# Performance work log

Hardware: AMD Instinct MI355X
Metric: run time of the kernel (lower is better)

The kernel has to match this reference:

```python
import jax, jax.numpy as jnp
import numpy as np

N = 200000          # active voxels
C = 128             # channels (in == out, required by final elementwise multiply)
GRID = (256, 256, 64)
EPS = 1e-5


def setup_inputs() -> dict:
    rng = np.random.default_rng(0)
    total = GRID[0] * GRID[1] * GRID[2]
    lin = rng.choice(total, size=N, replace=False)
    coords = np.stack(np.unravel_index(lin, GRID), axis=1).astype(np.int64)  # [N,3]
    # dense voxel -> row lookup table; sentinel N means 'no active voxel here'
    lut = np.full(total, N, dtype=np.int32)
    lut[lin] = np.arange(N, dtype=np.int32)
    nb = np.full((3, 2, N), N, dtype=np.int32)  # [axis, {prev,next}, N]
    hi = np.array(GRID) - 1
    for a in range(3):
        for s, off in enumerate((-1, 1)):
            c = coords.copy()
            c[:, a] += off
            valid = (c[:, a] >= 0) & (c[:, a] <= hi[a])
            cc = np.clip(c, 0, hi)
            lin_n = np.ravel_multi_index(tuple(cc.T), GRID)
            nb[a, s] = np.where(valid, lut[lin_n], N)
    kf, kw, kg, kb = jax.random.split(jax.random.key(0), 4)
    features = jax.random.normal(kf, (N, C), jnp.float32)
    W = jax.random.normal(kw, (3, 3, C, C), jnp.float32) * (1.0 / np.sqrt(3.0 * C))
    gamma = 1.0 + 0.1 * jax.random.normal(kg, (3, C), jnp.float32)
    beta = 0.1 * jax.random.normal(kb, (3, C), jnp.float32)
    return {"features": features, "nb_idx": jnp.asarray(nb), "W": W,
            "gamma": gamma, "beta": beta}


def reference(features, nb_idx, W, gamma, beta):
    # zero pad row: gathering sentinel index N yields a zero contribution
    xp = jnp.concatenate([features, jnp.zeros((1, C), features.dtype)], axis=0)
    acc = jnp.zeros_like(features)
    for a in range(3):  # three 1D decomposition axes (3x1x1, 1x3x1, 1x1x3)
        prev = xp[nb_idx[a, 0]]                      # [N,C]
        nxt = xp[nb_idx[a, 1]]                       # [N,C]
        out = prev @ W[a, 0] + features @ W[a, 1] + nxt @ W[a, 2]
        # BatchNorm1d (training-mode batch stats, biased variance)
        mu = out.mean(axis=0)
        var = out.var(axis=0)
        out = (out - mu) * jax.lax.rsqrt(var + EPS) * gamma[a] + beta[a]
        acc = acc + jax.nn.sigmoid(out)
    return acc * features
```

## Files before the change

kernel.cpp:

```cpp
#include <hip/hip_runtime.h>
#include <hip/hip_bf16.h>

#define NVOX 200000
#define CCH  128
#define KTOT 384
#define EPS_BN 1e-5f
#define PB   625
#define TPB  5

typedef __bf16 bf16x8 __attribute__((ext_vector_type(8)));
typedef float  floatx4 __attribute__((ext_vector_type(4)));

#define XBF_OFF    0ull
#define XBF_BYTES  ((size_t)(NVOX + 1) * CCH * 2)
#define WT_OFF     (XBF_OFF + XBF_BYTES)
#define WT_BYTES   ((size_t)3 * CCH * KTOT * 2)
#define OUTB_OFF   (WT_OFF + WT_BYTES)
#define OUTB_BYTES ((size_t)3 * NVOX * CCH * 2)
#define STATS_OFF  (OUTB_OFF + OUTB_BYTES)
#define STATS_BYTES ((size_t)3 * 2 * CCH * 4)

__global__ void k_prep_x(const float* __restrict__ xf, __bf16* __restrict__ xbf) {
    int idx = blockIdx.x * blockDim.x + threadIdx.x;
    const int total = (NVOX + 1) * 16;
    if (idx >= total) return;
    float v[8];
    if (idx < NVOX * 16) {
        const float4* p = (const float4*)xf + (size_t)idx * 2;
        float4 f0 = p[0], f1 = p[1];
        v[0] = f0.x; v[1] = f0.y; v[2] = f0.z; v[3] = f0.w;
        v[4] = f1.x; v[5] = f1.y; v[6] = f1.z; v[7] = f1.w;
    } else {
        #pragma unroll
        for (int j = 0; j < 8; ++j) v[j] = 0.0f;
    }
    bf16x8 o;
    #pragma unroll
    for (int j = 0; j < 8; ++j) o[j] = (__bf16)v[j];
    *((bf16x8*)xbf + idx) = o;
}

__global__ void k_prep_w(const float* __restrict__ W, __bf16* __restrict__ wt) {
    int idx = blockIdx.x * blockDim.x + threadIdx.x;
    if (idx >= 3 * CCH * KTOT) return;
    int k = idx % KTOT; int rem = idx / KTOT;
    int c = rem % CCH;  int a = rem / CCH;
    int s = k >> 7, k0 = k & 127;
    wt[idx] = (__bf16)W[(((size_t)(a * 3 + s) * CCH) + k0) * CCH + c];
}

__launch_bounds__(256, 2)
__global__ void k_gemm(const __bf16* __restrict__ xbf, const __bf16* __restrict__ wt,
                       const int* __restrict__ nb, __bf16* __restrict__ outb,
                       float* __restrict__ stats) {
    __shared__ __bf16 smem[64 * 392];
    __shared__ int s_pn[128];

    const int a    = blockIdx.y;
    const int tid  = threadIdx.x;
    const int w    = tid >> 6;
    const int lane = tid & 63;
    const int q    = lane >> 4;
    const int ln   = lane & 15;

    const __bf16* wbase = wt + (size_t)a * CCH * KTOT;
    bf16x8 B0[12], B1[12];
    #pragma unroll
    for (int ks = 0; ks < 12; ++ks) {
        B0[ks] = *(const bf16x8*)(wbase + (size_t)(w * 32 + ln) * KTOT + ks * 32 + q * 8);
        B1[ks] = *(const bf16x8*)(wbase + (size_t)(w * 32 + 16 + ln) * KTOT + ks * 32 + q * 8);
    }

    for (int ti = 0; ti < TPB; ++ti) {
        const int row0 = (blockIdx.x + ti * PB) * 64;

        __syncthreads();
        if (tid < 128)
            s_pn[tid] = nb[(size_t)(a * 2 + (tid >> 6)) * NVOX + row0 + (tid & 63)];
        __syncthreads();

        bf16x8 areg[12];
        #pragma unroll
        for (int it = 0; it < 12; ++it) {
            int cc  = it * 256 + tid;
            int r   = cc / 48;
            int seg = cc - r * 48;
            int src = seg >> 4, ch = seg & 15;
            int g = (src == 1) ? (row0 + r) : s_pn[(src >> 1) * 64 + r];
            areg[it] = *(const bf16x8*)(xbf + (size_t)g * CCH + ch * 8);
        }
        #pragma unroll
        for (int it = 0; it < 12; ++it) {
            int cc  = it * 256 + tid;
            int r   = cc / 48;
            int seg = cc - r * 48;
            *(bf16x8*)(&smem[r * 392 + seg * 8]) = areg[it];
        }
        __syncthreads();

        floatx4 acc0[4], acc1[4];
        #pragma unroll
        for (int mt = 0; mt < 4; ++mt)
            #pragma unroll
            for (int r = 0; r < 4; ++r) { acc0[mt][r] = 0.0f; acc1[mt][r] = 0.0f; }

        #pragma unroll
        for (int ks = 0; ks < 12; ++ks) {
            #pragma unroll
            for (int mt = 0; mt < 4; ++mt) {
                bf16x8 afr = *(const bf16x8*)(&smem[(mt * 16 + ln) * 392 + ks * 32 + q * 8]);
                acc0[mt] = __builtin_amdgcn_mfma_f32_16x16x32_bf16(afr, B0[ks], acc0[mt], 0, 0, 0);
                acc1[mt] = __builtin_amdgcn_mfma_f32_16x16x32_bf16(afr, B1[ks], acc1[mt], 0, 0, 0);
            }
        }

        {
            float s0 = 0.f, ss0 = 0.f, s1 = 0.f, ss1 = 0.f;
            #pragma unroll
            for (int mt = 0; mt < 4; ++mt)
                #pragma unroll
                for (int r = 0; r < 4; ++r) {
                    float v0 = acc0[mt][r]; s0 += v0; ss0 += v0 * v0;
                    float v1 = acc1[mt][r]; s1 += v1; ss1 += v1 * v1;
                }
            s0 += __shfl_xor(s0, 16); ss0 += __shfl_xor(ss0, 16);
            s0 += __shfl_xor(s0, 32); ss0 += __shfl_xor(ss0, 32);
            s1 += __shfl_xor(s1, 16); ss1 += __shfl_xor(ss1, 16);
            s1 += __shfl_xor(s1, 32); ss1 += __shfl_xor(ss1, 32);
            if (lane < 16) {
                int c0 = w * 32 + lane, c1 = w * 32 + 16 + lane;
                atomicAdd(&stats[a * 2 * CCH + c0], s0);
                atomicAdd(&stats[a * 2 * CCH + CCH + c0], ss0);
                atomicAdd(&stats[a * 2 * CCH + c1], s1);
                atomicAdd(&stats[a * 2 * CCH + CCH + c1], ss1);
            }
        }

        __syncthreads();
        #pragma unroll
        for (int mt = 0; mt < 4; ++mt) {
            #pragma unroll
            for (int r = 0; r < 4; ++r) {
                int rr = mt * 16 + q * 4 + r;
                smem[rr * 136 + w * 32 + ln]      = (__bf16)acc0[mt][r];
                smem[rr * 136 + w * 32 + 16 + ln] = (__bf16)acc1[mt][r];
            }
        }
        __syncthreads();
        #pragma unroll
        for (int it = 0; it < 4; ++it) {
            int i = it * 256 + tid;
            int r = i >> 4, ch = i & 15;
            bf16x8 v = *(const bf16x8*)(&smem[r * 136 + ch * 8]);
            *(bf16x8*)(outb + ((size_t)a * NVOX + row0 + r) * CCH + ch * 8) = v;
        }
    }
}

__launch_bounds__(256)
__global__ void k_final(const __bf16* __restrict__ outb, const float* __restrict__ xf,
                        const float* __restrict__ stats, const float* __restrict__ gamma,
                        const float* __restrict__ beta, float* __restrict__ out) {
    __shared__ float lsc[384], lsh[384];
    int tid = threadIdx.x;
    for (int i = tid; i < 384; i += 256) {
        int a = i >> 7, c = i & 127;
        float mu  = stats[a * 256 + c] * (1.0f / NVOX);
        float var = stats[a * 256 + 128 + c] * (1.0f / NVOX) - mu * mu;
        float rs  = rsqrtf(var + EPS_BN);
        float g = gamma[i], b = beta[i];
        lsc[i] = rs * g;
        lsh[i] = b - mu * rs * g;
    }
    __syncthreads();
    const int total = NVOX * 16;
    for (int idx = blockIdx.x * 256 + tid; idx < total; idx += gridDim.x * 256) {
        int c0 = (idx & 15) * 8;
        float4 f0 = ((const float4*)xf)[(size_t)idx * 2];
        float4 f1 = ((const float4*)xf)[(size_t)idx * 2 + 1];
        float r[8];
        #pragma unroll
        for (int j = 0; j < 8; ++j) r[j] = 0.0f;
        #pragma unroll
        for (int a = 0; a < 3; ++a) {
            bf16x8 o = *((const bf16x8*)outb + (size_t)a * NVOX * 16 + idx);
            #pragma unroll
            for (int j = 0; j < 8; ++j) {
                float v = (float)o[j] * lsc[a * 128 + c0 + j] + lsh[a * 128 + c0 + j];
                r[j] += __builtin_amdgcn_rcpf(1.0f + __expf(-v));
            }
        }
        float4 o0, o1;
        o0.x = r[0] * f0.x; o0.y = r[1] * f0.y; o0.z = r[2] * f0.z; o0.w = r[3] * f0.w;
        o1.x = r[4] * f1.x; o1.y = r[5] * f1.y; o1.z = r[6] * f1.z; o1.w = r[7] * f1.w;
        ((float4*)out)[(size_t)idx * 2]     = o0;
        ((float4*)out)[(size_t)idx * 2 + 1] = o1;
    }
}

extern "C" void kernel_launch(void* const* d_in, const int* in_sizes, int n_in,
                              void* d_out, int out_size, void* d_ws, size_t ws_size,
                              hipStream_t stream) {
    const float* xf    = (const float*)d_in[0];
    const int*   nb    = (const int*)  d_in[1];
    const float* W     = (const float*)d_in[2];
    const float* gamma = (const float*)d_in[3];
    const float* beta  = (const float*)d_in[4];
    float* out = (float*)d_out;

    char* ws = (char*)d_ws;
    __bf16* xbf   = (__bf16*)(ws + XBF_OFF);
    __bf16* wt    = (__bf16*)(ws + WT_OFF);
    __bf16* outb  = (__bf16*)(ws + OUTB_OFF);
    float*  stats = (float*)(ws + STATS_OFF);

    hipMemsetAsync(stats, 0, STATS_BYTES, stream);
    k_prep_x<<<((NVOX + 1) * 16 + 255) / 256, 256, 0, stream>>>(xf, xbf);
    k_prep_w<<<(3 * CCH * KTOT + 255) / 256, 256, 0, stream>>>(W, wt);
    k_gemm<<<dim3(PB, 3), 256, 0, stream>>>(xbf, wt, nb, outb, stats);
    k_final<<<2048, 256, 0, stream>>>(outb, xf, stats, gamma, beta, out);
}
```

Measured before the change: 415.5 us.

## Prefetch next tile's gathered rows during MFMA and defer BN stat atomics

```diff
diff --git a/kernel.cpp b/kernel.cpp
--- a/kernel.cpp
+++ b/kernel.cpp
@@ -53,8 +53,9 @@
 __global__ void k_gemm(const __bf16* __restrict__ xbf, const __bf16* __restrict__ wt,
                        const int* __restrict__ nb, __bf16* __restrict__ outb,
                        float* __restrict__ stats) {
-    __shared__ __bf16 smem[64 * 392];
-    __shared__ int s_pn[128];
+    __shared__ __bf16 smemA[64 * 392];
+    __shared__ __bf16 smemO[64 * 136];
+    __shared__ int s_pn[2][128];
 
     const int a    = blockIdx.y;
     const int tid  = threadIdx.x;
@@ -71,33 +72,63 @@
         B1[ks] = *(const bf16x8*)(wbase + (size_t)(w * 32 + 16 + ln) * KTOT + ks * 32 + q * 8);
     }
 
-    for (int ti = 0; ti < TPB; ++ti) {
-        const int row0 = (blockIdx.x + ti * PB) * 64;
-
-        __syncthreads();
-        if (tid < 128)
-            s_pn[tid] = nb[(size_t)(a * 2 + (tid >> 6)) * NVOX + row0 + (tid & 63)];
-        __syncthreads();
-
-        bf16x8 areg[12];
+    float s0 = 0.f, ss0 = 0.f, s1 = 0.f, ss1 = 0.f;
+
+    int r_pn = 0;
+    if (tid < 128) {
+        r_pn = nb[(size_t)(a * 2 + (tid >> 6)) * NVOX + blockIdx.x * 64 + (tid & 63)];
+        s_pn[0][tid] = r_pn;
+    }
+    __syncthreads();
+
+    bf16x8 areg[12];
+    {
+        const int row0 = blockIdx.x * 64;
         #pragma unroll
         for (int it = 0; it < 12; ++it) {
             int cc  = it * 256 + tid;
             int r   = cc / 48;
             int seg = cc - r * 48;
             int src = seg >> 4, ch = seg & 15;
-            int g = (src == 1) ? (row0 + r) : s_pn[(src >> 1) * 64 + r];
+            int g = (src == 1) ? (row0 + r) : s_pn[0][(src >> 1) * 64 + r];
             areg[it] = *(const bf16x8*)(xbf + (size_t)g * CCH + ch * 8);
         }
+    }
+    if (tid < 128)
+        r_pn = nb[(size_t)(a * 2 + (tid >> 6)) * NVOX + (blockIdx.x + PB) * 64 + (tid & 63)];
+
+    #pragma unroll
+    for (int ti = 0; ti < TPB; ++ti) {
+        const int row0 = (blockIdx.x + ti * PB) * 64;
+        const int buf  = ti & 1;
+
         #pragma unroll
         for (int it = 0; it < 12; ++it) {
             int cc  = it * 256 + tid;
             int r   = cc / 48;
             int seg = cc - r * 48;
-            *(bf16x8*)(&smem[r * 392 + seg * 8]) = areg[it];
-        }
+            *(bf16x8*)(&smemA[r * 392 + seg * 8]) = areg[it];
+        }
+        if (ti + 1 < TPB && tid < 128) s_pn[buf ^ 1][tid] = r_pn;
         __syncthreads();
 
+        bf16x8 areg2[12];
+        if (ti + 1 < TPB) {
+            const int rown = (blockIdx.x + (ti + 1) * PB) * 64;
+            #pragma unroll
+            for (int it = 0; it < 12; ++it) {
+                int cc  = it * 256 + tid;
+                int r   = cc / 48;
+                int seg = cc - r * 48;
+                int src = seg >> 4, ch = seg & 15;
+                int g = (src == 1) ? (rown + r) : s_pn[buf ^ 1][(src >> 1) * 64 + r];
+                areg2[it] = *(const bf16x8*)(xbf + (size_t)g * CCH + ch * 8);
+            }
+            if (ti + 2 < TPB && tid < 128)
+                r_pn = nb[(size_t)(a * 2 + (tid >> 6)) * NVOX
+                          + (blockIdx.x + (ti + 2) * PB) * 64 + (tid & 63)];
+        }
+
         floatx4 acc0[4], acc1[4];
         #pragma unroll
         for (int mt = 0; mt < 4; ++mt)
@@ -108,52 +139,55 @@
         for (int ks = 0; ks < 12; ++ks) {
             #pragma unroll
             for (int mt = 0; mt < 4; ++mt) {
-                bf16x8 afr = *(const bf16x8*)(&smem[(mt * 16 + ln) * 392 + ks * 32 + q * 8]);
+                bf16x8 afr = *(const bf16x8*)(&smemA[(mt * 16 + ln) * 392 + ks * 32 + q * 8]);
                 acc0[mt] = __builtin_amdgcn_mfma_f32_16x16x32_bf16(afr, B0[ks], acc0[mt], 0, 0, 0);
                 acc1[mt] = __builtin_amdgcn_mfma_f32_16x16x32_bf16(afr, B1[ks], acc1[mt], 0, 0, 0);
             }
         }
 
-        {
-            float s0 = 0.f, ss0 = 0.f, s1 = 0.f, ss1 = 0.f;
-            #pragma unroll
-            for (int mt = 0; mt < 4; ++mt)
-                #pragma unroll
-                for (int r = 0; r < 4; ++r) {
-                    float v0 = acc0[mt][r]; s0 += v0; ss0 += v0 * v0;
-                    float v1 = acc1[mt][r]; s1 += v1; ss1 += v1 * v1;
-                }
-            s0 += __shfl_xor(s0, 16); ss0 += __shfl_xor(ss0, 16);
-            s0 += __shfl_xor(s0, 32); ss0 += __shfl_xor(ss0, 32);
-            s1 += __shfl_xor(s1, 16); ss1 += __shfl_xor(ss1, 16);
-            s1 += __shfl_xor(s1, 32); ss1 += __shfl_xor(ss1, 32);
-            if (lane < 16) {
-                int c0 = w * 32 + lane, c1 = w * 32 + 16 + lane;
-                atomicAdd(&stats[a * 2 * CCH + c0], s0);
-                atomicAdd(&stats[a * 2 * CCH + CCH + c0], ss0);
-                atomicAdd(&stats[a * 2 * CCH + c1], s1);
-                atomicAdd(&stats[a * 2 * CCH + CCH + c1], ss1);
-            }
-        }
-
-        __syncthreads();
+        #pragma unroll
+        for (int mt = 0; mt < 4; ++mt)
+            #pragma unroll
+            for (int r = 0; r < 4; ++r) {
+                float v0 = acc0[mt][r]; s0 += v0; ss0 += v0 * v0;
+                float v1 = acc1[mt][r]; s1 += v1; ss1 += v1 * v1;
+            }
+
         #pragma unroll
         for (int mt = 0; mt < 4; ++mt) {
             #pragma unroll
             for (int r = 0; r < 4; ++r) {
                 int rr = mt * 16 + q * 4 + r;
-                smem[rr * 136 + w * 32 + ln]      = (__bf16)acc0[mt][r];
-                smem[rr * 136 + w * 32 + 16 + ln] = (__bf16)acc1[mt][r];
+                smemO[rr * 136 + w * 32 + ln]      = (__bf16)acc0[mt][r];
+                smemO[rr * 136 + w * 32 + 16 + ln] = (__bf16)acc1[mt][r];
             }
         }
         __syncthreads();
-        #pragma unroll
-        for (int it = 0; it < 4; ++it) {
-            int i = it * 256 + tid;
+
+        #pragma unroll
+        for (int it2 = 0; it2 < 4; ++it2) {
+            int i = it2 * 256 + tid;
             int r = i >> 4, ch = i & 15;
-            bf16x8 v = *(const bf16x8*)(&smem[r * 136 + ch * 8]);
+            bf16x8 v = *(const bf16x8*)(&smemO[r * 136 + ch * 8]);
             *(bf16x8*)(outb + ((size_t)a * NVOX + row0 + r) * CCH + ch * 8) = v;
         }
+
+        if (ti + 1 < TPB) {
+            #pragma unroll
+            for (int it = 0; it < 12; ++it) areg[it] = areg2[it];
+        }
+    }
+
+    s0 += __shfl_xor(s0, 16); ss0 += __shfl_xor(ss0, 16);
+    s0 += __shfl_xor(s0, 32); ss0 += __shfl_xor(ss0, 32);
+    s1 += __shfl_xor(s1, 16); ss1 += __shfl_xor(ss1, 16);
+    s1 += __shfl_xor(s1, 32); ss1 += __shfl_xor(ss1, 32);
+    if (lane < 16) {
+        int c0 = w * 32 + lane, c1 = w * 32 + 16 + lane;
+        atomicAdd(&stats[a * 2 * CCH + c0], s0);
+        atomicAdd(&stats[a * 2 * CCH + CCH + c0], ss0);
+        atomicAdd(&stats[a * 2 * CCH + c1], s1);
+        atomicAdd(&stats[a * 2 * CCH + CCH + c1], ss1);
     }
 }
 
```

After: 543.7 us. 1.31x slower.
